# Kernel tuning notes

Hardware: AMD Instinct MI355X
Metric: run time of the kernel (lower is better)

Reference implementation:

```python
import jax, jax.numpy as jnp
import numpy as np

N_ATOMS = 30000
N_PAIRS = 1200000
N_BASIS = 7
N_RADIAL = 5
N_SPECIES = 119
R_MIN = 0.5
R_MAX = 6.0
UNITS = (512, 512)
BOX = 6.0  # Angstrom box edge so many pairs fall inside the cutoff
N_FEAT = 360  # gaussian-moment feature count for n_radial=5

# static triangular index sets (fully symmetric contractions)
_TRI2_I, _TRI2_J = np.triu_indices(N_RADIAL)
_TRI3 = np.array([(i, j, k) for i in range(N_RADIAL)
                  for j in range(i, N_RADIAL)
                  for k in range(j, N_RADIAL)], dtype=np.int32)


def setup_inputs() -> dict:
    key = jax.random.key(0)
    ks = jax.random.split(key, 8)
    R = jax.random.uniform(ks[0], (N_ATOMS, 3), jnp.float32) * BOX
    Z = jax.random.randint(ks[1], (N_ATOMS,), 0, N_SPECIES, dtype=jnp.int32)
    idx = jax.random.randint(ks[2], (2, N_PAIRS), 0, N_ATOMS, dtype=jnp.int32)
    W_radial = jax.random.normal(ks[3], (N_SPECIES, N_SPECIES, N_RADIAL, N_BASIS), jnp.float32) / np.sqrt(N_BASIS)
    w1 = jax.random.normal(ks[4], (N_FEAT, UNITS[0]), jnp.float32) / np.sqrt(N_FEAT)
    b1 = jnp.zeros((UNITS[0],), jnp.float32)
    w2 = jax.random.normal(ks[5], (UNITS[0], UNITS[1]), jnp.float32) / np.sqrt(UNITS[0])
    b2 = jnp.zeros((UNITS[1],), jnp.float32)
    w3 = jax.random.normal(ks[6], (UNITS[1], 1), jnp.float32) / np.sqrt(UNITS[1])
    b3 = jnp.zeros((1,), jnp.float32)
    scale = 2.0 * jnp.ones((N_SPECIES, 1), jnp.float32)
    shift = 1.0 * jnp.ones((N_SPECIES, 1), jnp.float32)
    return dict(R=R, Z=Z, idx=idx, W_radial=W_radial, w1=w1, b1=b1,
                w2=w2, b2=b2, w3=w3, b3=b3, scale=scale, shift=shift)


def _descriptor(R, Z, idx, W_radial):
    idx_i, idx_j = idx[0], idx[1]
    # pairwise displacement (free-space displacement fn)
    dr_vec = R[idx_j] - R[idx_i]                                  # [P,3]
    dr = jnp.sqrt(jnp.sum(dr_vec * dr_vec, axis=-1) + 1e-12)      # [P]
    dn = dr_vec / (dr + 1e-5)[:, None]                            # unit vectors [P,3]

    # gaussian radial basis
    betta = N_BASIS ** 2 / R_MAX ** 2
    rad_norm = (2.0 * betta / np.pi) ** 0.25
    shifts = R_MIN + (R_MAX - R_MIN) / N_BASIS * jnp.arange(N_BASIS, dtype=jnp.float32)
    basis = rad_norm * jnp.exp(-betta * (dr[:, None] - shifts) ** 2)  # [P,B]

    # cosine cutoff and per species-pair embedding of the basis
    cutoff = 0.5 * (jnp.cos(jnp.pi * dr / R_MAX) + 1.0) * (dr < R_MAX)
    coeffs = W_radial[Z[idx_i], Z[idx_j]]                          # [P,K,B] irregular gather
    radial = jnp.einsum('pkb,pb->pk', coeffs, basis)               # [P,K]
    radial = radial * (cutoff / np.sqrt(N_BASIS))[:, None]

    seg = lambda x: jax.ops.segment_sum(x, idx_i, num_segments=N_ATOMS)
    # geometric moments of order 0..3
    m0 = seg(radial)                                               # [A,K]
    m1 = seg(radial[:, :, None] * dn[:, None, :])                  # [A,K,3]
    dn2 = dn[:, :, None] * dn[:, None, :]                          # [P,3,3]
    m2 = seg(radial[:, :, None, None] * dn2[:, None])              # [A,K,3,3]
    dn3 = dn2[:, :, :, None] * dn[:, None, None, :]                # [P,3,3,3]
    m3 = seg(radial[:, :, None, None, None] * dn3[:, None])        # [A,K,3,3,3]

    # gaussian-moment invariant contractions
    c1 = jnp.einsum('ari,asi->ars', m1, m1)
    c2 = jnp.einsum('arij,asij->ars', m2, m2)
    c3 = jnp.einsum('arijk,asijk->ars', m3, m3)
    c4 = jnp.einsum('arij,asik,atjk->arst', m2, m2, m2)
    c5 = jnp.einsum('ari,asj,atij->arst', m1, m1, m2)
    c6 = jnp.einsum('arijk,asijl,atkl->arst', m3, m3, m2)
    c7 = jnp.einsum('arijk,asij,atk->arst', m3, m2, m1)

    A = m0.shape[0]
    gm = jnp.concatenate([
        m0,
        c1[:, _TRI2_I, _TRI2_J],
        c2[:, _TRI2_I, _TRI2_J],
        c3[:, _TRI2_I, _TRI2_J],
        c4[:, _TRI3[:, 0], _TRI3[:, 1], _TRI3[:, 2]],
        c5[:, _TRI2_I, _TRI2_J, :].reshape(A, -1),
        c6[:, _TRI2_I, _TRI2_J, :].reshape(A, -1),
        c7.reshape(A, -1),
    ], axis=-1)                                                    # [A,360]
    return gm


def reference(R, Z, idx, W_radial, w1, b1, w2, b2, w3, b3, scale, shift):
    gm = _descriptor(R, Z, idx, W_radial)
    h = jax.nn.swish(gm @ w1 + b1)
    h = jax.nn.swish(h @ w2 + b2)
    h = h @ w3 + b3                                                # [A,1]
    return scale[Z] * h + shift[Z]
```

## Files before the change

kernel.cpp:

```cpp
#include <hip/hip_runtime.h>

#define NA      30000
#define MPAD    30080
#define NPAIRS  1200000
#define NB      7
#define NK      5
#define NSP     119
#define NFEAT   360
#define KP1     384
#define NU      512
#define WROWH   40
#define MAXSLOT 120
#define PSTRIDE 128
#define NBKF    235
#define BCAPF   5760
#define PPB     4688
#define NTILE   235

#define BETTA      1.3611111111111112f
#define RADNORM    0.96481348f
#define SHIFT_STEP 0.7857142857142857f
#define PI_OVER_R  0.5235987755982988f
#define INV_SQRT7  0.3779644730092272f
#define RMAXV      6.0f
#define TCOEF      2.138888888888889f

typedef __attribute__((ext_vector_type(8))) short bf16x8;
typedef __attribute__((ext_vector_type(4))) float f32x4;
typedef __attribute__((ext_vector_type(2))) float f32x2;
typedef __attribute__((ext_vector_type(4))) unsigned int u32x4;
typedef _Float16 h16x2 __attribute__((ext_vector_type(2)));

__device__ __forceinline__ unsigned short f2b(float x) {
    unsigned u = __float_as_uint(x);
    unsigned r = u + 0x7FFF + ((u >> 16) & 1);
    return (unsigned short)(r >> 16);
}

__global__ __launch_bounds__(256)
void k_part(const int* __restrict__ idx, const int* __restrict__ Z,
            int* __restrict__ gcur, int* __restrict__ part) {
    __shared__ int hist[NBKF];
    __shared__ int base[NBKF];
    int tid = threadIdx.x;
    for (int b = tid; b < NBKF; b += 256) hist[b] = 0;
    __syncthreads();
    int p0 = blockIdx.x * PPB;
    int p1 = min(p0 + PPB, NPAIRS);
    for (int p = p0 + tid; p < p1; p += 256)
        atomicAdd(&hist[idx[p] >> 7], 1);
    __syncthreads();
    for (int b = tid; b < NBKF; b += 256) {
        base[b] = atomicAdd(&gcur[b], hist[b]);
        hist[b] = 0;
    }
    __syncthreads();
    for (int p = p0 + tid; p < p1; p += 256) {
        int i = idx[p];
        int b = i >> 7;
        int j = idx[NPAIRS + p];
        int zj = Z[j];
        int off = base[b] + atomicAdd(&hist[b], 1);
        if (off < BCAPF)
            part[b * BCAPF + off] = ((i & 127) << 22) | (zj << 15) | j;
    }
}

__global__ __launch_bounds__(256)
void k_csr(const int* __restrict__ part, const int* __restrict__ gcnt,
           int* __restrict__ counts, int* __restrict__ plist) {
    __shared__ int lp[128 * MAXSLOT];
    __shared__ int lc[128];
    int tid = threadIdx.x;
    int lane = tid & 63, wave = tid >> 6;
    int w = blockIdx.x;
    for (int t = tid; t < 128; t += 256) lc[t] = 0;
    __syncthreads();
    int n = min(gcnt[w], BCAPF);
    for (int e = tid; e < n; e += 256) {
        int v = part[w * BCAPF + e];
        int i7 = v >> 22;
        int r = atomicAdd(&lc[i7], 1);
        if (r < MAXSLOT) lp[i7 * MAXSLOT + r] = v & 0x3FFFFF;
    }
    __syncthreads();
    for (int t = tid; t < 128; t += 256) {
        int a = w * 128 + t;
        if (a < NA) counts[a] = min(lc[t], MAXSLOT);
    }
    for (int rr = 0; rr < 32; rr++) {
        int row = wave * 32 + rr;
        int a = w * 128 + row;
        if (a < NA) {
            int n_r = min(lc[row], MAXSLOT);
            for (int c = lane; c < n_r; c += 64)
                plist[(size_t)a * PSTRIDE + c] = lp[row * MAXSLOT + c];
        }
    }
}

#define PREP_W   (NSP*NSP*WROWH)
#define PREP_R   NA
#define PREP_W1  (NU*KP1)
#define PREP_W2  (NU*NU)
#define PREP_TOT (PREP_W + PREP_R + PREP_W1 + PREP_W2)
__global__ void k_prep(const float* __restrict__ W, const float* __restrict__ R,
                       const float* __restrict__ w1, const float* __restrict__ w2,
                       unsigned short* __restrict__ Wp, float* __restrict__ Rp,
                       unsigned short* __restrict__ w1T, unsigned short* __restrict__ w2T,
                       int* __restrict__ gcur, float* __restrict__ out) {
    int i = blockIdx.x * blockDim.x + threadIdx.x;
    if (i < 256) gcur[i] = 0;
    if (i < NA) out[i] = 0.f;
    if (i < PREP_W) {
        int row = i / WROWH, e = i - row * WROWH;
        int k = e >> 3, b = e & 7;
        float v = (b < 7) ? W[row * (NK * NB) + k * NB + b] : 0.f;
        ((_Float16*)Wp)[i] = (_Float16)v;
        return;
    }
    i -= PREP_W;
    if (i < PREP_R) {
        f32x4 v = {R[3*i], R[3*i+1], R[3*i+2], 0.f};
        *(f32x4*)&Rp[4*i] = v;
        return;
    }
    i -= PREP_R;
    if (i < PREP_W1) {
        int c = i / KP1, kp = i - c * KP1;
        w1T[i] = (kp < NFEAT) ? f2b(w1[kp * NU + c]) : (unsigned short)0;
        return;
    }
    i -= PREP_W1;
    if (i < PREP_W2) {
        int c = i >> 9, kp = i & 511;
        w2T[i] = f2b(w2[kp * NU + c]);
    }
}

#define LDM(comp) M[(comp) * 65]

__device__ __forceinline__ void do_c5(const float* M, unsigned short* STrow,
                                      int r, int s, int foff) {
    const int S2[3][3] = {{0,1,2},{1,3,4},{2,4,5}};
    float m1r[3], m1q[3];
#pragma unroll
    for (int i = 0; i < 3; i++) m1r[i] = LDM(r*20+1+i);
#pragma unroll
    for (int i = 0; i < 3; i++) m1q[i] = LDM(s*20+1+i);
    float pre[9];
#pragma unroll
    for (int i = 0; i < 3; i++)
#pragma unroll
        for (int j = 0; j < 3; j++) pre[i*3+j] = m1r[i] * m1q[j];
    for (int t = 0; t < 5; t++) {
        float m2t[6];
#pragma unroll
        for (int u = 0; u < 6; u++) m2t[u] = LDM(t*20+4+u);
        float v = 0.f;
#pragma unroll
        for (int i = 0; i < 3; i++)
#pragma unroll
            for (int j = 0; j < 3; j++)
                v += pre[i*3+j] * m2t[S2[i][j]];
        STrow[foff + t] = f2b(v);
    }
}

__device__ __forceinline__ void do_c6(const float* M, unsigned short* STrow,
                                      int r, int s, int foff) {
    const int S2[3][3] = {{0,1,2},{1,3,4},{2,4,5}};
    const int S3[3][3][3] = {
        {{0,1,2},{1,3,4},{2,4,5}},
        {{1,3,4},{3,6,7},{4,7,8}},
        {{2,4,5},{4,7,8},{5,8,9}}
    };
    float m3r[10];
#pragma unroll
    for (int u = 0; u < 10; u++) m3r[u] = LDM(r*20+10+u);
    float m2q[6];
#pragma unroll
    for (int u = 0; u < 6; u++) m2q[u] = LDM(s*20+4+u);
    float U0 = 0.f, U1 = 0.f, U2 = 0.f;
#pragma unroll
    for (int i = 0; i < 3; i++)
#pragma unroll
        for (int j = 0; j < 3; j++) {
            float ww = m2q[S2[i][j]];
            U0 += m3r[S3[i][j][0]] * ww;
            U1 += m3r[S3[i][j][1]] * ww;
            U2 += m3r[S3[i][j][2]] * ww;
        }
    for (int t = 0; t < 5; t++) {
        float v = U0 * LDM(t*20+1) + U1 * LDM(t*20+2) + U2 * LDM(t*20+3);
        STrow[foff + t] = f2b(v);
    }
}

__device__ __forceinline__ void do_c7(const float* M, unsigned short* STrow,
                                      int r, int s, int foff) {
    const int S2[3][3] = {{0,1,2},{1,3,4},{2,4,5}};
    const int S3[3][3][3] = {
        {{0,1,2},{1,3,4},{2,4,5}},
        {{1,3,4},{3,6,7},{4,7,8}},
        {{2,4,5},{4,7,8},{5,8,9}}
    };
    float m3r[10], m3q[10];
#pragma unroll
    for (int u = 0; u < 10; u++) m3r[u] = LDM(r*20+10+u);
#pragma unroll
    for (int u = 0; u < 10; u++) m3q[u] = LDM(s*20+10+u);
    float T[3][3];
#pragma unroll
    for (int k = 0; k < 3; k++)
#pragma unroll
        for (int l = 0; l < 3; l++) {
            float v = 0.f;
#pragma unroll
            for (int i = 0; i < 3; i++)
#pragma unroll
                for (int j = 0; j < 3; j++)
                    v += m3r[S3[i][j][k]] * m3q[S3[i][j][l]];
            T[k][l] = v;
        }
    for (int t = 0; t < 5; t++) {
        float m2t[6];
#pragma unroll
        for (int u = 0; u < 6; u++) m2t[u] = LDM(t*20+4+u);
        float v = 0.f;
#pragma unroll
        for (int k = 0; k < 3; k++)
#pragma unroll
            for (int l = 0; l < 3; l++)
                v += T[k][l] * m2t[S2[k][l]];
        STrow[foff + t] = f2b(v);
    }
}

__global__ __launch_bounds__(512, 2)
void k_momcon(const float* __restrict__ Rp, const int* __restrict__ Z,
              const unsigned short* __restrict__ WpH, const int* __restrict__ counts,
              const int* __restrict__ plist, unsigned short* __restrict__ gmB) {
    __shared__ float MS[100 * 65];
    __shared__ __align__(4) unsigned short ST[64 * 242];
    int tid = threadIdx.x;
    int g = tid >> 3, q = tid & 7;
    int a0 = blockIdx.x * 64;
    int a = a0 + g;

    if (a < NA) {
        f32x4 ri = *(const f32x4*)&Rp[4*a];
        int Zi = Z[a];
        f32x2 acc[50];
#pragma unroll
        for (int u = 0; u < 50; u++) acc[u] = (f32x2){0.f, 0.f};
        int cnt = min(counts[a], MAXSLOT);
        const int* prow = plist + (size_t)a * PSTRIDE;

        const float DCH[6] = {0.14812156f, 0.027590652f, 0.0051393300f,
                              0.00095730500f, 0.00017831700f, 3.3215300e-05f};

        int pk0 = prow[q & 127];
        int pk1 = prow[(q + 8) & 127];
        int j0c = min(pk0 & 0x7FFF, NA - 1);
        f32x4 rj = *(const f32x4*)&Rp[4 * j0c];

        for (int t = q; t < cnt; t += 8) {
            int pk2 = prow[(t + 16) & 127];
            int j1c = min(pk1 & 0x7FFF, NA - 1);
            f32x4 rjn = *(const f32x4*)&Rp[4 * j1c];

            int Zj = (pk0 >> 15) & 0x7F;
            const u32x4* wv = (const u32x4*)(WpH + (size_t)(Zi * NSP + Zj) * WROWH);
            u32x4 wv0 = wv[0], wv1 = wv[1], wv2 = wv[2], wv3 = wv[3], wv4 = wv[4];
            unsigned wu[20];
#pragma unroll
            for (int c = 0; c < 4; c++) {
                wu[c]      = wv0[c];
                wu[4 + c]  = wv1[c];
                wu[8 + c]  = wv2[c];
                wu[12 + c] = wv3[c];
                wu[16 + c] = wv4[c];
            }

            float dx = rj.x - ri.x, dy = rj.y - ri.y, dz = rj.z - ri.z;
            float d2 = dx*dx + dy*dy + dz*dz + 1e-12f;
            float dr = sqrtf(d2);
            float inv = 1.0f / (dr + 1e-5f);
            float nx = dx*inv, ny = dy*inv, nz = dz*inv;

            float t0 = dr - 0.5f;
            float bb[NB];
            bb[0] = RADNORM * __expf(-BETTA * t0 * t0);
            float Tg = __expf(TCOEF * dr);
#pragma unroll
            for (int b = 0; b < 6; b++) bb[b+1] = bb[b] * Tg * DCH[b];

            float cut = (dr < RMAXV) ? 0.5f * (__cosf(PI_OVER_R * dr) + 1.0f) : 0.0f;
            cut *= INV_SQRT7;

            h16x2 bp[4];
            bp[0] = (h16x2){(_Float16)bb[0], (_Float16)bb[1]};
            bp[1] = (h16x2){(_Float16)bb[2], (_Float16)bb[3]};
            bp[2] = (h16x2){(_Float16)bb[4], (_Float16)bb[5]};
            bp[3] = (h16x2){(_Float16)bb[6], (_Float16)0.0f};

            float rad[NK];
#pragma unroll
            for (int k = 0; k < NK; k++) {
                float s = 0.f;
#if __has_builtin(__builtin_amdgcn_fdot2)
#pragma unroll
                for (int c = 0; c < 4; c++)
                    s = __builtin_amdgcn_fdot2(
                        __builtin_bit_cast(h16x2, wu[k*4 + c]), bp[c], s, false);
#else
#pragma unroll
                for (int c = 0; c < 4; c++) {
                    h16x2 w = __builtin_bit_cast(h16x2, wu[k*4 + c]);
                    s += (float)w.x * (float)bp[c].x + (float)w.y * (float)bp[c].y;
                }
#endif
                rad[k] = s * cut;
            }

            float gg[20];
            gg[0] = 1.f; gg[1] = nx; gg[2] = ny; gg[3] = nz;
            gg[4] = nx*nx; gg[5] = nx*ny; gg[6] = nx*nz; gg[7] = ny*ny; gg[8] = ny*nz; gg[9] = nz*nz;
            gg[10] = gg[4]*nx; gg[11] = gg[4]*ny; gg[12] = gg[4]*nz; gg[13] = gg[5]*ny; gg[14] = gg[5]*nz;
            gg[15] = gg[6]*nz; gg[16] = gg[7]*ny; gg[17] = gg[7]*nz; gg[18] = gg[8]*nz; gg[19] = gg[9]*nz;
            f32x2 g2[10];
#pragma unroll
            for (int u = 0; u < 10; u++) g2[u] = (f32x2){gg[2*u], gg[2*u+1]};
#pragma unroll
            for (int k = 0; k < NK; k++) {
                f32x2 rk = (f32x2){rad[k], rad[k]};
#pragma unroll
                for (int u = 0; u < 10; u++)
                    acc[k*10 + u] += rk * g2[u];
            }
            pk0 = pk1; pk1 = pk2; rj = rjn;
        }
#pragma unroll
        for (int u = 0; u < 50; u++) {
            f32x2 v = acc[u];
            double d = __builtin_bit_cast(double, v);
            d = __shfl_xor(d, 1);
            v += __builtin_bit_cast(f32x2, d);
            d = __builtin_bit_cast(double, v);
            d = __shfl_xor(d, 2);
            v += __builtin_bit_cast(f32x2, d);
            d = __builtin_bit_cast(double, v);
            d = __shfl_xor(d, 4);
            v += __builtin_bit_cast(f32x2, d);
            acc[u] = v;
        }
        if (q == 0) {
#pragma unroll
            for (int u = 0; u < 50; u++) {
                MS[(2*u)     * 65 + g] = acc[u].x;
                MS[(2*u + 1) * 65 + g] = acc[u].y;
            }
        }
    }
    __syncthreads();

    int lane = tid & 63, wave = tid >> 6;
    const float* M = MS + lane;
    unsigned short* STrow = ST + lane * 242;

    if (wave == 0) {
        for (int k = 0; k < 5; k++) STrow[k] = f2b(LDM(k * 20));
        int f = 5;
        for (int r = 0; r < 5; r++)
            for (int s = r; s < 5; s++) {
                float v = 0.f;
#pragma unroll
                for (int i = 0; i < 3; i++) v += LDM(r*20+1+i) * LDM(s*20+1+i);
                STrow[f++] = f2b(v);
            }
        const float W2U[6] = {1,2,2,1,2,1};
        for (int r = 0; r < 5; r++)
            for (int s = r; s < 5; s++) {
                float v = 0.f;
#pragma unroll
                for (int u = 0; u < 6; u++) v += W2U[u] * LDM(r*20+4+u) * LDM(s*20+4+u);
                STrow[f++] = f2b(v);
            }
        const float W3U[10] = {1,3,3,3,6,3,1,3,3,1};
        for (int r = 0; r < 5; r++)
            for (int s = r; s < 5; s++) {
                float v = 0.f;
#pragma unroll
                for (int u = 0; u < 10; u++) v += W3U[u] * LDM(r*20+10+u) * LDM(s*20+10+u);
                STrow[f++] = f2b(v);
            }
        do_c7(M, STrow, 3, 4, 160 + 13*5);
        do_c7(M, STrow, 4, 4, 160 + 14*5);
    } else if (wave == 1 || wave == 2) {
        const int S2[3][3] = {{0,1,2},{1,3,4},{2,4,5}};
        int e0 = (wave == 1) ? 0 : 18, e1 = (wave == 1) ? 18 : 35;
        int e = 0;
        for (int r = 0; r < 5; r++)
            for (int s = r; s < 5; s++)
                for (int t = s; t < 5; t++) {
                    if (e >= e0 && e < e1) {
                        float m2r[6], m2q[6], m2t[6];
#pragma unroll
                        for (int u = 0; u < 6; u++) m2r[u] = LDM(r*20+4+u);
#pragma unroll
                        for (int u = 0; u < 6; u++) m2q[u] = LDM(s*20+4+u);
#pragma unroll
                        for (int u = 0; u < 6; u++) m2t[u] = LDM(t*20+4+u);
                        float v = 0.f;
#pragma unroll
                        for (int i = 0; i < 3; i++)
#pragma unroll
                            for (int j = 0; j < 3; j++)
#pragma unroll
                                for (int k = 0; k < 3; k++)
                                    v += m2r[S2[i][j]] * m2q[S2[i][k]] * m2t[S2[j][k]];
                        STrow[50 + e] = f2b(v);
                    }
                    e++;
                }
    } else if (wave == 3) {
        int p = 0;
        for (int r = 0; r < 5; r++)
            for (int s = r; s < 5; s++) {
                if (p < 8) do_c5(M, STrow, r, s, 85 + p*5);
                p++;
            }
        do_c7(M, STrow, 3, 3, 160 + 12*5);
    } else if (wave == 4) {
        int p = 0;
        for (int r = 0; r < 5; r++)
            for (int s = r; s < 5; s++) {
                if (p >= 8) do_c5(M, STrow, r, s, 85 + p*5);
                p++;
            }
        do_c6(M, STrow, 0, 0, 235);
    } else {
        int pc0 = (wave - 5) * 4;
        int p = 0;
        for (int r = 0; r < 5; r++)
            for (int s = r; s < 5; s++) {
                if (p >= pc0 && p < pc0 + 4) do_c7(M, STrow, r, s, 160 + p*5);
                p++;
            }
    }
    __syncthreads();
    for (int e = tid; e < 64 * 120; e += 512) {
        int row = e / 120, c = e - row * 120;
        if (a0 + row < NA)
            *(unsigned int*)&gmB[(size_t)(a0 + row) * KP1 + 2*c] =
                *(const unsigned int*)&ST[row * 242 + 2*c];
    }
    __syncthreads();

    {
        int g0 = 1 + wave * 3;
        for (int gi = 0; gi < 3; gi++) {
            int gr = g0 + gi;
            int r = gr / 5, s = gr - r * 5;
            do_c6(M, STrow, r, s, 235 + gr*5 - 240);
        }
        if (wave == 0) {
            for (int z = 360; z < 384; z++) STrow[z - 240] = 0;
        }
    }
    __syncthreads();
    for (int e = tid; e < 64 * 72; e += 512) {
        int row = e / 72, c = e - row * 72;
        if (a0 + row < NA)
            *(unsigned int*)&gmB[(size_t)(a0 + row) * KP1 + 240 + 2*c] =
                *(const unsigned int*)&ST[row * 242 + 2*c];
    }
}

__device__ __forceinline__ void stage8(const unsigned short* gp, unsigned short* lp) {
    __builtin_amdgcn_global_load_lds(
        (const __attribute__((address_space(1))) unsigned int*)gp,
        (__attribute__((address_space(3))) unsigned int*)lp, 16, 0, 0);
}

template<int KPAD, int MODE>
__global__ __launch_bounds__(256) void k_mfma(const unsigned short* __restrict__ A,
                                              const unsigned short* __restrict__ B,
                                              const float* __restrict__ bias,
                                              const float* __restrict__ w3,
                                              void* __restrict__ outp) {
    __shared__ __align__(16) unsigned char SMEM[35072];
    unsigned short* As = (unsigned short*)SMEM;
    unsigned short* Bs = (unsigned short*)(SMEM + 16384);
    float* red = (float*)(SMEM + 32768);
    int tid = threadIdx.x;
    int lane = tid & 63, wave = tid >> 6;
    int wm = wave >> 1, wn = wave & 1;
    int quad = lane >> 4, l16 = lane & 15;
    int lrow = lane >> 3;
    int lchk = lane & 7;

    int bid = blockIdx.x;
    int xcd = bid & 7, rr_ = bid >> 3;
    int cblk = rr_ & 3, agrp = rr_ >> 2;
    int atile = xcd * 30 + agrp;
    if (atile >= NTILE) return;

    int rowA0, rowB0;
    if (MODE == 1) { rowA0 = atile * 128; rowB0 = cblk * 128; }
    else           { rowA0 = cblk * 128;  rowB0 = atile * 128; }

    f32x4 acc[4][4];
    f32x4 zero = {0.f, 0.f, 0.f, 0.f};
#pragma unroll
    for (int i = 0; i < 4; i++)
#pragma unroll
        for (int j = 0; j < 4; j++) acc[i][j] = zero;

    for (int k0 = 0; k0 < KPAD; k0 += 64) {
        __syncthreads();
#pragma unroll
        for (int i = 0; i < 4; i++) {
            int r = wave * 32 + i * 8 + lrow;
            int gc = lchk ^ (r & 7);
            stage8(A + (size_t)(rowA0 + r) * KPAD + k0 + gc * 8, &As[(wave * 32 + i * 8) * 64]);
        }
#pragma unroll
        for (int i = 0; i < 4; i++) {
            int r = wave * 32 + i * 8 + lrow;
            int gc = lchk ^ (r & 7);
            stage8(B + (size_t)(rowB0 + r) * KPAD + k0 + gc * 8, &Bs[(wave * 32 + i * 8) * 64]);
        }
        __syncthreads();
#pragma unroll
        for (int s = 0; s < 2; s++) {
            bf16x8 af[4], bfr[4];
#pragma unroll
            for (int mt = 0; mt < 4; mt++) {
                int r = wm * 64 + mt * 16 + l16;
                af[mt] = *(const bf16x8*)&As[r * 64 + (((s * 4 + quad) ^ (r & 7)) * 8)];
            }
#pragma unroll
            for (int nt = 0; nt < 4; nt++) {
                int r = wn * 64 + nt * 16 + l16;
                bfr[nt] = *(const bf16x8*)&Bs[r * 64 + (((s * 4 + quad) ^ (r & 7)) * 8)];
            }
#pragma unroll
            for (int mt = 0; mt < 4; mt++)
#pragma unroll
                for (int nt = 0; nt < 4; nt++)
                    acc[mt][nt] = __builtin_amdgcn_mfma_f32_16x16x32_bf16(
                        af[mt], bfr[nt], acc[mt][nt], 0, 0, 0);
        }
    }

    if (MODE == 1) {
        __syncthreads();
        unsigned short* Ot = (unsigned short*)SMEM;
#pragma unroll
        for (int nt = 0; nt < 4; nt++) {
            int c_loc = wn * 64 + nt * 16 + l16;
            float b = bias[rowB0 + c_loc];
#pragma unroll
            for (int mt = 0; mt < 4; mt++) {
#pragma unroll
                for (int reg = 0; reg < 4; reg++) {
                    int a_loc = wm * 64 + mt * 16 + quad * 4 + reg;
                    float v = acc[mt][nt][reg] + b;
                    Ot[a_loc * 136 + c_loc] = f2b(v / (1.f + __expf(-v)));
                }
            }
        }
        __syncthreads();
        unsigned short* O = (unsigned short*)outp;
        int half = lane >> 5, l32 = lane & 31;
#pragma unroll
        for (int it = 0; it < 16; it++) {
            int rloc = wave * 32 + it * 2 + half;
            int a = rowA0 + rloc;
            unsigned long long d = *(const unsigned long long*)&Ot[rloc * 136 + l32 * 4];
            if (a < NA)
                *(unsigned long long*)&O[(size_t)a * NU + rowB0 + l32 * 4] = d;
        }
    } else {
        float pn[4] = {0.f, 0.f, 0.f, 0.f};
#pragma unroll
        for (int mt = 0; mt < 4; mt++) {
#pragma unroll
            for (int reg = 0; reg < 4; reg++) {
                int c = rowA0 + wm * 64 + mt * 16 + quad * 4 + reg;
                float b = bias[c];
                float w3c = w3[c];
#pragma unroll
                for (int nt = 0; nt < 4; nt++) {
                    float v = acc[mt][nt][reg] + b;
                    pn[nt] += w3c * (v / (1.f + __expf(-v)));
                }
            }
        }
#pragma unroll
        for (int nt = 0; nt < 4; nt++) {
            pn[nt] += __shfl_xor(pn[nt], 16);
            pn[nt] += __shfl_xor(pn[nt], 32);
        }
        __syncthreads();
        if (quad == 0) {
#pragma unroll
            for (int nt = 0; nt < 4; nt++)
                red[((wm * 2 + wn) * 4 + nt) * 16 + l16] = pn[nt];
        }
        __syncthreads();
        if (tid < 128) {
            int wn2 = tid >> 6, nt2 = (tid >> 4) & 3, lb = tid & 15;
            float s = red[((0 * 2 + wn2) * 4 + nt2) * 16 + lb]
                    + red[((1 * 2 + wn2) * 4 + nt2) * 16 + lb];
            int a = rowB0 + wn2 * 64 + nt2 * 16 + lb;
            if (a < NA) atomicAdd((float*)outp + a, s);
        }
    }
}

__global__ void k_finish(float* __restrict__ out, const float* __restrict__ b3,
                         const int* __restrict__ Z, const float* __restrict__ scale,
                         const float* __restrict__ shift) {
    int a = blockIdx.x * blockDim.x + threadIdx.x;
    if (a >= NA) return;
    int z = Z[a];
    out[a] = scale[z] * (out[a] + b3[0]) + shift[z];
}

extern "C" void kernel_launch(void* const* d_in, const int* in_sizes, int n_in,
                              void* d_out, int out_size, void* d_ws, size_t ws_size,
                              hipStream_t stream) {
    const float* R    = (const float*)d_in[0];
    const int*   Z    = (const int*)  d_in[1];
    const int*   idx  = (const int*)  d_in[2];
    const float* Wr   = (const float*)d_in[3];
    const float* w1   = (const float*)d_in[4];
    const float* b1   = (const float*)d_in[5];
    const float* w2   = (const float*)d_in[6];
    const float* b2   = (const float*)d_in[7];
    const float* w3   = (const float*)d_in[8];
    const float* b3   = (const float*)d_in[9];
    const float* scale= (const float*)d_in[10];
    const float* shift= (const float*)d_in[11];
    float* out = (float*)d_out;
    char* ws = (char*)d_ws;

    int*            gcur   = (int*)  (ws + 0);
    int*            counts = (int*)  (ws + 1024);
    int*            part   = (int*)  (ws + 121024);
    int*            plist  = (int*)  (ws + 5558016);
    unsigned short* gmB    = (unsigned short*)(ws + 32918016);
    unsigned short* w1T    = (unsigned short*)(ws + 56019456);
    unsigned short* w2T    = (unsigned short*)(ws + 56412672);
    unsigned short* h1B    = (unsigned short*)(ws + 56936960);
    unsigned short* WpH    = (unsigned short*)(ws + 87738880);
    float*          Rpad   = (float*)(ws + 89778064);

    k_prep   <<<(PREP_TOT + 255) / 256, 256, 0, stream>>>(Wr, R, w1, w2, WpH, Rpad,
                                                          w1T, w2T, gcur, out);
    k_part   <<<256, 256, 0, stream>>>(idx, Z, gcur, part);
    k_csr    <<<NBKF, 256, 0, stream>>>(part, gcur, counts, plist);
    k_momcon <<<(NA + 63) / 64, 512, 0, stream>>>(Rpad, Z, WpH, counts, plist, gmB);

    k_mfma<KP1, 1><<<960, 256, 0, stream>>>(gmB, w1T, b1, nullptr, (void*)h1B);
    k_mfma<NU,  2><<<960, 256, 0, stream>>>(w2T, h1B, b2, w3, (void*)out);

    k_finish<<<(NA + 255) / 256, 256, 0, stream>>>(out, b3, Z, scale, shift);
}
```

Measured before the change: 239.6 us.

## Fuse CSR bucket build into moment kernel using shared-memory pair lists

```diff
diff --git a/kernel.cpp b/kernel.cpp
--- a/kernel.cpp
+++ b/kernel.cpp
@@ -11,7 +11,6 @@
 #define NU      512
 #define WROWH   40
 #define MAXSLOT 120
-#define PSTRIDE 128
 #define NBKF    235
 #define BCAPF   5760
 #define PPB     4688
@@ -63,39 +62,6 @@
         int off = base[b] + atomicAdd(&hist[b], 1);
         if (off < BCAPF)
             part[b * BCAPF + off] = ((i & 127) << 22) | (zj << 15) | j;
-    }
-}
-
-__global__ __launch_bounds__(256)
-void k_csr(const int* __restrict__ part, const int* __restrict__ gcnt,
-           int* __restrict__ counts, int* __restrict__ plist) {
-    __shared__ int lp[128 * MAXSLOT];
-    __shared__ int lc[128];
-    int tid = threadIdx.x;
-    int lane = tid & 63, wave = tid >> 6;
-    int w = blockIdx.x;
-    for (int t = tid; t < 128; t += 256) lc[t] = 0;
-    __syncthreads();
-    int n = min(gcnt[w], BCAPF);
-    for (int e = tid; e < n; e += 256) {
-        int v = part[w * BCAPF + e];
-        int i7 = v >> 22;
-        int r = atomicAdd(&lc[i7], 1);
-        if (r < MAXSLOT) lp[i7 * MAXSLOT + r] = v & 0x3FFFFF;
-    }
-    __syncthreads();
-    for (int t = tid; t < 128; t += 256) {
-        int a = w * 128 + t;
-        if (a < NA) counts[a] = min(lc[t], MAXSLOT);
-    }
-    for (int rr = 0; rr < 32; rr++) {
-        int row = wave * 32 + rr;
-        int a = w * 128 + row;
-        if (a < NA) {
-            int n_r = min(lc[row], MAXSLOT);
-            for (int c = lane; c < n_r; c += 64)
-                plist[(size_t)a * PSTRIDE + c] = lp[row * MAXSLOT + c];
-        }
     }
 }
 
@@ -239,13 +205,35 @@
 
 __global__ __launch_bounds__(512, 2)
 void k_momcon(const float* __restrict__ Rp, const int* __restrict__ Z,
-              const unsigned short* __restrict__ WpH, const int* __restrict__ counts,
-              const int* __restrict__ plist, unsigned short* __restrict__ gmB) {
-    __shared__ float MS[100 * 65];
-    __shared__ __align__(4) unsigned short ST[64 * 242];
+              const unsigned short* __restrict__ WpH, const int* __restrict__ gcnt,
+              const int* __restrict__ part, unsigned short* __restrict__ gmB) {
+    __shared__ __align__(16) unsigned char LDSM[59024];
+    float* MS = (float*)LDSM;
+    int* lp = (int*)(LDSM + 26000);
+    unsigned short* ST = (unsigned short*)(LDSM + 26000);
+    int* lc = (int*)(LDSM + 58768);
     int tid = threadIdx.x;
+    int a0 = blockIdx.x * 64;
+
+    {
+        int bkt = blockIdx.x >> 1;
+        int half = blockIdx.x & 1;
+        for (int t = tid; t < 64; t += 512) lc[t] = 0;
+        __syncthreads();
+        int n = min(gcnt[bkt], BCAPF);
+        for (int e = tid; e < n; e += 512) {
+            int v = part[bkt * BCAPF + e];
+            int i7 = v >> 22;
+            if ((i7 >> 6) == half) {
+                int i6 = i7 & 63;
+                int r = atomicAdd(&lc[i6], 1);
+                if (r < MAXSLOT) lp[i6 * 128 + r] = v & 0x3FFFFF;
+            }
+        }
+        __syncthreads();
+    }
+
     int g = tid >> 3, q = tid & 7;
-    int a0 = blockIdx.x * 64;
     int a = a0 + g;
 
     if (a < NA) {
@@ -254,8 +242,8 @@
         f32x2 acc[50];
 #pragma unroll
         for (int u = 0; u < 50; u++) acc[u] = (f32x2){0.f, 0.f};
-        int cnt = min(counts[a], MAXSLOT);
-        const int* prow = plist + (size_t)a * PSTRIDE;
+        int cnt = min(lc[g], MAXSLOT);
+        const int* prow = lp + g * 128;
 
         const float DCH[6] = {0.14812156f, 0.027590652f, 0.0051393300f,
                               0.00095730500f, 0.00017831700f, 3.3215300e-05f};
@@ -649,9 +637,7 @@
     char* ws = (char*)d_ws;
 
     int*            gcur   = (int*)  (ws + 0);
-    int*            counts = (int*)  (ws + 1024);
     int*            part   = (int*)  (ws + 121024);
-    int*            plist  = (int*)  (ws + 5558016);
     unsigned short* gmB    = (unsigned short*)(ws + 32918016);
     unsigned short* w1T    = (unsigned short*)(ws + 56019456);
     unsigned short* w2T    = (unsigned short*)(ws + 56412672);
@@ -662,8 +648,7 @@
     k_prep   <<<(PREP_TOT + 255) / 256, 256, 0, stream>>>(Wr, R, w1, w2, WpH, Rpad,
                                                           w1T, w2T, gcur, out);
     k_part   <<<256, 256, 0, stream>>>(idx, Z, gcur, part);
-    k_csr    <<<NBKF, 256, 0, stream>>>(part, gcur, counts, plist);
-    k_momcon <<<(NA + 63) / 64, 512, 0, stream>>>(Rpad, Z, WpH, counts, plist, gmB);
+    k_momcon <<<(NA + 63) / 64, 512, 0, stream>>>(Rpad, Z, WpH, gcur, part, gmB);
 
     k_mfma<KP1, 1><<<960, 256, 0, stream>>>(gmB, w1T, b1, nullptr, (void*)h1B);
     k_mfma<NU,  2><<<960, 256, 0, stream>>>(w2T, h1B, b2, w3, (void*)out);
```

New measurement: 233.5 us. -2.5%, faster.
